# Performance work log

Hardware: AMD Instinct MI355X
Metric: run time of the kernel (lower is better)

## Reference

```python
import jax, jax.numpy as jnp
import numpy as np

B, N, E, D = 2, 4096, 1024, 128  # batch, seq, embed_dim, expand_ratio (head dim)
H = E // D                        # 8 heads
LN_EPS = 1e-5


def setup_inputs() -> dict:
    key = jax.random.key(0)
    ks = jax.random.split(key, 6)
    s = 0.02
    return {
        "x": jax.random.normal(ks[0], (B, N, E), jnp.float32),
        "W_in": jax.random.normal(ks[1], (3 * E, E), jnp.float32) * s,
        "W_out": jax.random.normal(ks[2], (E, E), jnp.float32) * s,
        "W_g1": jax.random.normal(ks[3], (D, E), jnp.float32) * s,
        "W_g2": jax.random.normal(ks[4], (E, D), jnp.float32) * s,
        "ln_w": jnp.ones((E,), jnp.float32),
    }


def _gla_scan(q, k, v, g):
    # q,k,v,g: [b,h,n,d]; GLA recurrence: S_t = exp(g_t)[:,None]*S_{t-1} + k_t v_t^T; o_t = q_t @ S_t
    def step(S, inp):
        qt, kt, vt, gt = inp  # each [b,h,d]
        S = jnp.exp(gt)[..., None] * S + kt[..., None] * vt[..., None, :]  # [b,h,d,d]
        ot = jnp.einsum('bhd,bhde->bhe', qt, S)
        return S, ot

    xs = tuple(jnp.moveaxis(a, 2, 0) for a in (q, k, v, g))  # [n,b,h,d]
    S0 = jnp.zeros(q.shape[:2] + (q.shape[-1], v.shape[-1]), q.dtype)
    _, o = jax.lax.scan(step, S0, xs)
    return jnp.moveaxis(o, 0, 2)  # [b,h,n,d]


def reference(x, W_in, W_out, W_g1, W_g2, ln_w):
    b, n, e = x.shape
    u = x @ W_in.T                       # [b,n,3E]
    v, q, lg = jnp.split(u, 3, axis=-1)  # note order: v, q, log_f
    q = jax.nn.silu(q)                   # q_activation = silu
    f = jax.nn.sigmoid(lg)
    k = 1.0 - f                          # non_sparse_ratio == 1 path
    g = jax.nn.log_sigmoid(lg)           # log of forget gate

    def tohead(a):
        return a.reshape(b, n, H, D).transpose(0, 2, 1, 3)  # b h n d

    o = _gla_scan(tohead(q), tohead(k), tohead(v), tohead(g))
    o = o.transpose(0, 2, 1, 3).reshape(b, n, e)  # b n (h d)

    gate = jax.nn.sigmoid((x @ W_g1.T) @ W_g2.T)  # low-rank output gate
    o = o * gate

    mu = jnp.mean(o, axis=-1, keepdims=True)
    var = jnp.var(o, axis=-1, keepdims=True)
    o = (o - mu) * jax.lax.rsqrt(var + LN_EPS) * ln_w  # layernorm, no bias
    return o @ W_out.T
```

## Files before the change

kernel.cpp:

```cpp
#include <hip/hip_runtime.h>
#include <cmath>

#define B_ 2
#define N_ 4096
#define E_ 1024
#define D_ 128
#define H_ 8
#define CHUNK 64
#define NC_ (N_/CHUNK)
#define UW_ (3*E_ + D_)

__device__ __forceinline__ float sigmoidf_(float x){ return 1.f/(1.f + __expf(-x)); }

__device__ __forceinline__ unsigned short f2bf(float f){
    unsigned u = __float_as_uint(f);
    u += 0x7FFFu + ((u >> 16) & 1u);
    return (unsigned short)(u >> 16);
}
__device__ __forceinline__ float bf2f(unsigned short s){
    return __uint_as_float(((unsigned)s) << 16);
}
__device__ __forceinline__ unsigned short f2bf_fast(float f){
    __bf16 h = (__bf16)f;
    return __builtin_bit_cast(unsigned short, h);
}

typedef __attribute__((ext_vector_type(8))) __bf16 bf16x8;
typedef __attribute__((ext_vector_type(4))) float  f32x4;
typedef __attribute__((address_space(3))) unsigned int as3_u32;
typedef __attribute__((address_space(1))) unsigned int as1_u32;

__device__ __forceinline__ void gload_lds16(const void* g, void* l){
    __builtin_amdgcn_global_load_lds((as1_u32*)g, (as3_u32*)l, 16, 0, 0);
}

__device__ __forceinline__ bf16x8 ldsfrag256(const unsigned short* Lp, int row, int kg){
    return *reinterpret_cast<const bf16x8*>(&Lp[row*128 + ((kg ^ (row&7))<<3)]);
}
__device__ __forceinline__ bf16x8 ldsfrag128(const unsigned short* Lp, int row, int kg){
    return *reinterpret_cast<const bf16x8*>(&Lp[row*64 + ((kg ^ (row&7))<<3)]);
}
__device__ __forceinline__ bf16x8 u4_to_bf(uint4 u){
    return __builtin_bit_cast(bf16x8, u);
}

template<bool OUT_BF16>
__global__ __launch_bounds__(256) void gemm_bf16(
    const unsigned short* __restrict__ A,
    const unsigned short* __restrict__ Bw,
    void* __restrict__ Cout, int M, int N, int K, int lda)
{
    __shared__ unsigned short As[128*64];
    __shared__ unsigned short Bs[128*64];
    const int tid  = threadIdx.x;
    const int wave = tid >> 6;
    const int lane = tid & 63;
    const int gx = gridDim.x;
    const int nwg = gx * gridDim.y;
    int bid = blockIdx.y*gx + blockIdx.x;
    bid = (bid & 7)*(nwg >> 3) + (bid >> 3);
    const int m0 = (bid / gx) * 128, n0 = (bid % gx) * 128;
    const int wr = (wave >> 1) * 64;
    const int wc = (wave & 1) * 64;
    const int l15 = lane & 15, l4 = lane >> 4;
    const int p = l15 & 7;

    f32x4 acc[4][4];
#pragma unroll
    for (int i=0;i<4;i++)
#pragma unroll
        for (int j=0;j<4;j++)
#pragma unroll
            for (int q=0;q<4;q++) acc[i][j][q]=0.f;

    const int srow = wave*32 + (lane>>3);
    const int sgrp = lane & 7;

    for (int k0=0; k0<K; k0+=64){
        if (k0) __syncthreads();
#pragma unroll
        for (int i=0;i<4;i++){
            const int r  = srow + 8*i;
            const int cg = sgrp ^ (r & 7);
            gload_lds16(A  + (size_t)(m0 + r)*lda + k0 + cg*8, &As[(wave*32 + 8*i)*64]);
            gload_lds16(Bw + (size_t)(n0 + r)*K   + k0 + cg*8, &Bs[(wave*32 + 8*i)*64]);
        }
        __syncthreads();
#pragma unroll
        for (int ks=0; ks<2; ks++){
            bf16x8 av[4], bv[4];
            const int tA = (((ks<<2) | l4) ^ p) << 3;
#pragma unroll
            for (int f=0; f<4; f++){
                const int rowA = wr + f*16 + l15;
                const int rowB = wc + f*16 + l15;
                av[f] = *reinterpret_cast<const bf16x8*>(&As[(rowA<<6) + tA]);
                bv[f] = *reinterpret_cast<const bf16x8*>(&Bs[(rowB<<6) + tA]);
            }
#pragma unroll
            for (int fm=0; fm<4; fm++)
#pragma unroll
                for (int fn=0; fn<4; fn++)
                    acc[fm][fn] = __builtin_amdgcn_mfma_f32_16x16x32_bf16(
                        av[fm], bv[fn], acc[fm][fn], 0, 0, 0);
        }
    }
    const int crow0 = m0 + wr + l4*4;
    const int ccol0 = n0 + wc + l15;
    if (!OUT_BF16){
        float* C = (float*)Cout;
#pragma unroll
        for (int fm=0; fm<4; fm++)
#pragma unroll
            for (int fn=0; fn<4; fn++)
#pragma unroll
                for (int j=0;j<4;j++)
                    C[(size_t)(crow0 + fm*16 + j)*N + ccol0 + fn*16] = acc[fm][fn][j];
    } else {
        unsigned short* C = (unsigned short*)Cout;
#pragma unroll
        for (int fm=0; fm<4; fm++)
#pragma unroll
            for (int fn=0; fn<4; fn++)
#pragma unroll
                for (int j=0;j<4;j++)
                    C[(size_t)(crow0 + fm*16 + j)*N + ccol0 + fn*16] = f2bf(acc[fm][fn][j]);
    }
}

#define CQX 2097152
#define WQ1 786432
#define WQ3 32768
#define WQ2 262144
#define WQ4 32768
__global__ __launch_bounds__(256) void cast_all(
    const float* __restrict__ x,
    const float* __restrict__ w1, const float* __restrict__ w3,
    const float* __restrict__ w2, const float* __restrict__ w4,
    unsigned short* __restrict__ xb, unsigned short* __restrict__ wcat,
    unsigned short* __restrict__ w2b, unsigned short* __restrict__ w4b)
{
    const int total = CQX+WQ1+WQ3+WQ2+WQ4;
    for (int i = blockIdx.x*256 + threadIdx.x; i < total; i += gridDim.x*256){
        const float* src; unsigned short* dst; int off;
        if (i < CQX){ src=x; dst=xb; off=i; }
        else if (i < CQX+WQ1){ src=w1; dst=wcat; off=i-CQX; }
        else if (i < CQX+WQ1+WQ3){ src=w3; dst=wcat+WQ1*4; off=i-CQX-WQ1; }
        else if (i < CQX+WQ1+WQ3+WQ2){ src=w2; dst=w2b; off=i-CQX-WQ1-WQ3; }
        else { src=w4; dst=w4b; off=i-CQX-WQ1-WQ3-WQ2; }
        const float4 v = reinterpret_cast<const float4*>(src)[off];
        ushort4 o;
        o.x = f2bf(v.x); o.y = f2bf(v.y); o.z = f2bf(v.z); o.w = f2bf(v.w);
        reinterpret_cast<ushort4*>(dst)[off] = o;
    }
}

__global__ __launch_bounds__(512) void gla_prep(
    const unsigned short* __restrict__ u, float* __restrict__ EBC,
    unsigned short* __restrict__ QSb, unsigned short* __restrict__ KINb,
    unsigned short* __restrict__ KINtb, unsigned short* __restrict__ Vtb)
{
    __shared__ float tot[4*128];
    const int bid = blockIdx.x;
    const int c  = bid % NC_;
    const int hh = (bid / NC_) % H_;
    const int b  = bid / (NC_*H_);
    const int d  = threadIdx.x & 127;
    const int qd = threadIdx.x >> 7;
    const int t0 = qd*16;
    const size_t urow0 = ((size_t)b*N_ + (size_t)c*CHUNK)*UW_ + (size_t)hh*D_ + d;

    float bl[16], qv[16], vv[16];
#pragma unroll
    for (int i=0;i<16;i++)
        bl[i] = bf2f(u[urow0 + (size_t)(t0+i)*UW_ + 2*E_]);
#pragma unroll
    for (int i=0;i<16;i++)
        qv[i] = bf2f(u[urow0 + (size_t)(t0+i)*UW_ + E_]);
#pragma unroll
    for (int i=0;i<16;i++)
        vv[i] = bf2f(u[urow0 + (size_t)(t0+i)*UW_]);

    float acc = 0.f;
#pragma unroll
    for (int i=0;i<16;i++){
        const float lg = bl[i];
        const float e  = __expf(-fabsf(lg));
        const float g  = fminf(lg, 0.f) - __logf(1.f + e);
        acc += g;
        bl[i] = acc;
    }
    tot[qd*128 + d] = acc;
    __syncthreads();
    const float s0 = tot[d], s1 = tot[128+d], s2 = tot[256+d], s3 = tot[384+d];
    const float off = (qd>0 ? s0 : 0.f) + (qd>1 ? s1 : 0.f) + (qd>2 ? s2 : 0.f);
    const float bcv = s0 + s1 + s2 + s3;
    const float ebc = __expf(bcv);
    if (threadIdx.x < 128) EBC[(size_t)bid*D_ + d] = ebc;

    unsigned kin_pk[8], v_pk[8];
    float prev = 0.f;
    const size_t obase = (size_t)bid*CHUNK*D_;
#pragma unroll
    for (int i=0;i<16;i++){
        const int t = t0 + i;
        const float Bl = bl[i];
        const float g  = Bl - prev;  prev = Bl;
        const float Bc = Bl + off;
        const float kk = 1.f - __expf(g);
        const float eB = __expf(Bc);
        const float q  = qv[i];
        const float es = __expf(-q);
        const float silu = q * __builtin_amdgcn_rcpf(1.f + es);
        const float qs  = silu * eB;
        const float kin = kk * __builtin_amdgcn_rcpf(eB);
        QSb [obase + (size_t)t*D_ + d] = f2bf_fast(qs);
        KINb[obase + (size_t)t*D_ + d] = f2bf_fast(kin);
        const unsigned kb = f2bf_fast(kin * ebc);
        const unsigned vb = f2bf_fast(vv[i]);
        if (i & 1){ kin_pk[i>>1] |= kb<<16; v_pk[i>>1] |= vb<<16; }
        else      { kin_pk[i>>1]  = kb;     v_pk[i>>1]  = vb;     }
    }
    const size_t tbase = (size_t)bid*D_*CHUNK + (size_t)d*CHUNK + t0;
#pragma unroll
    for (int j=0;j<2;j++){
        uint4 kq, vq;
        kq.x=kin_pk[4*j]; kq.y=kin_pk[4*j+1]; kq.z=kin_pk[4*j+2]; kq.w=kin_pk[4*j+3];
        vq.x=v_pk[4*j];   vq.y=v_pk[4*j+1];   vq.z=v_pk[4*j+2];   vq.w=v_pk[4*j+3];
        *reinterpret_cast<uint4*>(&KINtb[tbase + j*8]) = kq;
        *reinterpret_cast<uint4*>(&Vtb  [tbase + j*8]) = vq;
    }
}

__global__ __launch_bounds__(256) void gla_chunk_mm(
    const unsigned short* __restrict__ Vtb,
    const unsigned short* __restrict__ KINtb,
    unsigned short* __restrict__ McTb)
{
    __shared__ unsigned short As[128*64];
    __shared__ unsigned short Bs[128*64];
    const int bid = blockIdx.x;
    const int tid = threadIdx.x;
    const int w = tid >> 6, lane = tid & 63;
    const int l15 = lane & 15, l4 = lane >> 4;
    const int wr = (w >> 1) * 64, wc = (w & 1) * 64;
    const unsigned short* A  = Vtb   + (size_t)bid*128*64;
    const unsigned short* Bp = KINtb + (size_t)bid*128*64;

    f32x4 acc[4][4];
#pragma unroll
    for (int i=0;i<4;i++)
#pragma unroll
        for (int j=0;j<4;j++)
#pragma unroll
            for (int q=0;q<4;q++) acc[i][j][q]=0.f;

#pragma unroll
    for (int i=0;i<4;i++){
        const int r  = w*32 + i*8 + (lane>>3);
        const int gs = (lane&7) ^ (r&7);
        gload_lds16(A  + (size_t)r*64 + gs*8, &As[(w*32+i*8)*64]);
        gload_lds16(Bp + (size_t)r*64 + gs*8, &Bs[(w*32+i*8)*64]);
    }
    __syncthreads();
#pragma unroll
    for (int ks=0; ks<2; ks++){
        bf16x8 av[4], bv[4];
#pragma unroll
        for (int f=0; f<4; f++){
            av[f] = ldsfrag128(As, wr + f*16 + l15, ks*4 + l4);
            bv[f] = ldsfrag128(Bs, wc + f*16 + l15, ks*4 + l4);
        }
#pragma unroll
        for (int fm=0; fm<4; fm++)
#pragma unroll
            for (int fn=0; fn<4; fn++)
                acc[fm][fn] = __builtin_amdgcn_mfma_f32_16x16x32_bf16(
                    av[fm], bv[fn], acc[fm][fn], 0, 0, 0);
    }
    unsigned short* C = McTb + (size_t)bid*128*128;
#pragma unroll
    for (int fm=0; fm<4; fm++)
#pragma unroll
        for (int fn=0; fn<4; fn++)
#pragma unroll
            for (int j=0;j<4;j++)
                C[(size_t)(wr + fm*16 + l4*4 + j)*128 + wc + fn*16 + l15] = f2bf(acc[fm][fn][j]);
}

__global__ __launch_bounds__(256) void gla_scan_chunks(
    const unsigned short* __restrict__ McTb, const float* __restrict__ EBC,
    unsigned short* __restrict__ Sb16)
{
    const size_t F = (size_t)blockIdx.x*256 + threadIdx.x;
    const int bh = (int)(F >> 14);
    const int rem = (int)(F & 16383);
    const int d = rem & 127;
    float S = 0.f;
    for (int c=0;c<NC_;c++){
        const size_t idx = (((size_t)bh*NC_ + c) << 14) + rem;
        const float m = bf2f(McTb[idx]);
        const float dec = EBC[((size_t)bh*NC_ + c)*D_ + d];
        Sb16[idx] = f2bf(S);
        S = dec*S + m;
    }
}

__global__ __launch_bounds__(256) void gla_output(
    const unsigned short* __restrict__ QSb,
    const unsigned short* __restrict__ KINb,
    const unsigned short* __restrict__ Vtb,
    const unsigned short* __restrict__ Sb,
    const unsigned short* __restrict__ G2b,
    unsigned short* __restrict__ Opre)
{
    __shared__ unsigned short QS_l[64*128];
    __shared__ unsigned short A_l [64*64];
    const int bid = blockIdx.x;
    const int c = bid % NC_;
    const int h = (bid / NC_) % H_;
    const int b = bid / (NC_*H_);
    const int tid = threadIdx.x;
    const int w = tid >> 6, lane = tid & 63;
    const int l15 = lane & 15, l4 = lane >> 4;

    const unsigned short* qb = QSb + (size_t)bid*64*128;
    const unsigned short* kb = KINb + (size_t)bid*64*128;
    const unsigned short* vb = Vtb + (size_t)bid*128*64;
    const unsigned short* sb = Sb  + (size_t)bid*128*128;

#pragma unroll
    for (int i=0;i<4;i++){
        const int r  = w*16 + i*4 + (lane>>4);
        const int gs = (lane&15) ^ (r&7);
        gload_lds16(qb + (size_t)r*128 + gs*8, &QS_l[(w*16+i*4)*128]);
    }
    uint4 kinr[4];
    {
        const int srow = w*16 + l15;
#pragma unroll
        for (int ks=0; ks<4; ks++)
            kinr[ks] = *reinterpret_cast<const uint4*>(kb + (size_t)srow*128 + (ks*4 + l4)*8);
    }
    __syncthreads();

    uint4 vtr[2][2], sr[2][4];
#pragma unroll
    for (int fe=0; fe<2; fe++){
        const int row = w*32 + fe*16 + l15;
#pragma unroll
        for (int ks=0; ks<2; ks++)
            vtr[fe][ks] = *reinterpret_cast<const uint4*>(vb + (size_t)row*64 + (ks*4 + l4)*8);
#pragma unroll
        for (int ks=0; ks<4; ks++)
            sr[fe][ks]  = *reinterpret_cast<const uint4*>(sb + (size_t)row*128 + (ks*4 + l4)*8);
    }

    f32x4 accA[4];
#pragma unroll
    for (int i=0;i<4;i++)
#pragma unroll
        for (int q=0;q<4;q++) accA[i][q]=0.f;
#pragma unroll
    for (int ks=0; ks<4; ks++){
        const bf16x8 bv = u4_to_bf(kinr[ks]);
#pragma unroll
        for (int ft=0; ft<4; ft++){
            const bf16x8 av = ldsfrag256(QS_l, ft*16 + l15, ks*4 + l4);
            accA[ft] = __builtin_amdgcn_mfma_f32_16x16x32_bf16(av, bv, accA[ft], 0,0,0);
        }
    }
#pragma unroll
    for (int ft=0; ft<4; ft++)
#pragma unroll
        for (int j=0;j<4;j++){
            const int t = ft*16 + l4*4 + j;
            const int s = w*16 + l15;
            const float vA = (t >= s) ? accA[ft][j] : 0.f;
            A_l[t*64 + (((s>>3) ^ (t&7))<<3) + (s&7)] = f2bf(vA);
        }
    __syncthreads();

    f32x4 acc[4][2];
#pragma unroll
    for (int i=0;i<4;i++)
#pragma unroll
        for (int j=0;j<2;j++)
#pragma unroll
            for (int q=0;q<4;q++) acc[i][j][q]=0.f;
#pragma unroll
    for (int ks=0; ks<2; ks++){
        const bf16x8 b0 = u4_to_bf(vtr[0][ks]);
        const bf16x8 b1 = u4_to_bf(vtr[1][ks]);
#pragma unroll
        for (int ft=0; ft<4; ft++){
            const bf16x8 av = ldsfrag128(A_l, ft*16 + l15, ks*4 + l4);
            acc[ft][0] = __builtin_amdgcn_mfma_f32_16x16x32_bf16(av, b0, acc[ft][0], 0,0,0);
            acc[ft][1] = __builtin_amdgcn_mfma_f32_16x16x32_bf16(av, b1, acc[ft][1], 0,0,0);
        }
    }
#pragma unroll
    for (int ks=0; ks<4; ks++){
        const bf16x8 b0 = u4_to_bf(sr[0][ks]);
        const bf16x8 b1 = u4_to_bf(sr[1][ks]);
#pragma unroll
        for (int ft=0; ft<4; ft++){
            const bf16x8 av = ldsfrag256(QS_l, ft*16 + l15, ks*4 + l4);
            acc[ft][0] = __builtin_amdgcn_mfma_f32_16x16x32_bf16(av, b0, acc[ft][0], 0,0,0);
            acc[ft][1] = __builtin_amdgcn_mfma_f32_16x16x32_bf16(av, b1, acc[ft][1], 0,0,0);
        }
    }
    const size_t rowbase = (size_t)b*N_ + (size_t)c*CHUNK;
#pragma unroll
    for (int ft=0; ft<4; ft++)
#pragma unroll
        for (int fe=0; fe<2; fe++)
#pragma unroll
            for (int j=0;j<4;j++){
                const int t = ft*16 + l4*4 + j;
                const int e = w*32 + fe*16 + l15;
                const size_t idx = (rowbase + t)*E_ + h*D_ + e;
                const float g = sigmoidf_(bf2f(G2b[idx]));
                Opre[idx] = f2bf(acc[ft][fe][j] * g);
            }
}

__global__ __launch_bounds__(256) void ln_bf16(
    const unsigned short* __restrict__ O, const float* __restrict__ lnw,
    unsigned short* __restrict__ Ob)
{
    const int row = blockIdx.x;
    const int tid = threadIdx.x;
    const size_t off = (size_t)row*E_ + tid*4;
    const ushort4 ov = *reinterpret_cast<const ushort4*>(&O[off]);
    float4 o;
    o.x = bf2f(ov.x); o.y = bf2f(ov.y); o.z = bf2f(ov.z); o.w = bf2f(ov.w);
    float s1 = o.x+o.y+o.z+o.w;
    float s2 = o.x*o.x + o.y*o.y + o.z*o.z + o.w*o.w;
#pragma unroll
    for (int sh=32; sh>0; sh>>=1){
        s1 += __shfl_down(s1, sh);
        s2 += __shfl_down(s2, sh);
    }
    __shared__ float r1[4], r2[4];
    const int wid = tid >> 6;
    if ((tid & 63)==0){ r1[wid]=s1; r2[wid]=s2; }
    __syncthreads();
    s1 = r1[0]+r1[1]+r1[2]+r1[3];
    s2 = r2[0]+r2[1]+r2[2]+r2[3];
    const float mean = s1 * (1.f/E_);
    const float var  = s2 * (1.f/E_) - mean*mean;
    const float rs   = rsqrtf(var + 1e-5f);
    const float4 w = *reinterpret_cast<const float4*>(&lnw[tid*4]);
    ushort4 r;
    r.x = f2bf((o.x-mean)*rs*w.x); r.y = f2bf((o.y-mean)*rs*w.y);
    r.z = f2bf((o.z-mean)*rs*w.z); r.w = f2bf((o.w-mean)*rs*w.w);
    *reinterpret_cast<ushort4*>(&Ob[off]) = r;
}

extern "C" void kernel_launch(void* const* d_in, const int* in_sizes, int n_in,
                              void* d_out, int out_size, void* d_ws, size_t ws_size,
                              hipStream_t stream)
{
    const float* x     = (const float*)d_in[0];
    const float* W_in  = (const float*)d_in[1];
    const float* W_out = (const float*)d_in[2];
    const float* W_g1  = (const float*)d_in[3];
    const float* W_g2  = (const float*)d_in[4];
    const float* lnw   = (const float*)d_in[5];
    float* out = (float*)d_out;
    char* ws = (char*)d_ws;

    unsigned short* ub2    = (unsigned short*)(ws);
    unsigned short* McTb   = (unsigned short*)(ws);
    unsigned short* Sb16   = (unsigned short*)(ws + 33554432);
    unsigned short* G2b    = (unsigned short*)(ws + 67108864);
    float*          EBC    = (float*)(ws + 100663296);
    unsigned short* QSb    = (unsigned short*)(ws + 101187584);
    unsigned short* KINb   = (unsigned short*)(ws + 117964800);
    unsigned short* KINtb  = (unsigned short*)(ws + 134742016);
    unsigned short* Vtb    = (unsigned short*)(ws + 151519232);
    unsigned short* Opre   = (unsigned short*)(ws + 168296448);
    unsigned short* xb     = (unsigned short*)(ws + 185073664);
    unsigned short* Wcatb  = (unsigned short*)(ws + 201850880);
    unsigned short* W_outb = (unsigned short*)(ws + 224919552);
    unsigned short* W_g2b  = (unsigned short*)(ws + 227278848);
    unsigned short* ObF    = (unsigned short*)(ws + 229638144);

    const int M = B_*N_;
    dim3 blk(256);

    cast_all<<<2048, blk, 0, stream>>>(x, W_in, W_g1, W_out, W_g2,
                                       xb, Wcatb, W_outb, W_g2b);

    gemm_bf16<true><<<dim3(UW_/128, M/128), blk, 0, stream>>>(
        xb, Wcatb, ub2, M, UW_, E_, E_);
    gla_prep<<<dim3(B_*H_*NC_), dim3(512), 0, stream>>>(ub2, EBC, QSb, KINb, KINtb, Vtb);
    gemm_bf16<true><<<dim3(E_/128, M/128), blk, 0, stream>>>(
        ub2 + 3*E_, W_g2b, G2b, M, E_, D_, UW_);
    gla_chunk_mm<<<dim3(B_*H_*NC_), blk, 0, stream>>>(Vtb, KINtb, McTb);
    gla_scan_chunks<<<dim3((B_*H_*D_*D_)/256), blk, 0, stream>>>(McTb, EBC, Sb16);
    gla_output<<<dim3(B_*H_*NC_), blk, 0, stream>>>(QSb, KINb, Vtb, Sb16, G2b, Opre);
    ln_bf16<<<dim3(M), blk, 0, stream>>>(Opre, lnw, ObF);
    gemm_bf16<false><<<dim3(E_/128, M/128), blk, 0, stream>>>(
        ObF, W_outb, out, M, E_, E_, E_);
}
```

Before: 195.0 us.

## Fuse low-rank gate GEMM into GLA output kernel and vectorize chunk scan

Removes the separate gate GEMM that wrote a bf16 gate tensor. The gla_output kernel now computes the gate's second projection in place with MFMA, reading the rank-128 projection from ub2 and W_g2. The chunk scan kernel now handles four state elements per thread with vector loads and stores, using a quarter of the blocks. The workspace is relaid out so ub2 is no longer aliased by McTb, since ub2 must survive until gla_output; this adds per-block MFMA work and uncoalesced global fragment loads.

```diff
diff --git a/kernel.cpp b/kernel.cpp
--- a/kernel.cpp
+++ b/kernel.cpp
@@ -292,17 +292,24 @@
     const unsigned short* __restrict__ McTb, const float* __restrict__ EBC,
     unsigned short* __restrict__ Sb16)
 {
-    const size_t F = (size_t)blockIdx.x*256 + threadIdx.x;
-    const int bh = (int)(F >> 14);
-    const int rem = (int)(F & 16383);
-    const int d = rem & 127;
-    float S = 0.f;
+    const int F4 = blockIdx.x*256 + threadIdx.x;
+    const int e4 = F4 << 2;
+    const int bh = e4 >> 14;
+    const int rem = e4 & 16383;
+    const int d0 = rem & 127;
+    float S0=0.f, S1=0.f, S2=0.f, S3=0.f;
     for (int c=0;c<NC_;c++){
         const size_t idx = (((size_t)bh*NC_ + c) << 14) + rem;
-        const float m = bf2f(McTb[idx]);
-        const float dec = EBC[((size_t)bh*NC_ + c)*D_ + d];
-        Sb16[idx] = f2bf(S);
-        S = dec*S + m;
+        const ushort4 m4 = *reinterpret_cast<const ushort4*>(&McTb[idx]);
+        const float4 dec = *reinterpret_cast<const float4*>(
+            &EBC[(((size_t)bh*NC_ + c) << 7) + d0]);
+        ushort4 s4;
+        s4.x = f2bf(S0); s4.y = f2bf(S1); s4.z = f2bf(S2); s4.w = f2bf(S3);
+        *reinterpret_cast<ushort4*>(&Sb16[idx]) = s4;
+        S0 = dec.x*S0 + bf2f(m4.x);
+        S1 = dec.y*S1 + bf2f(m4.y);
+        S2 = dec.z*S2 + bf2f(m4.z);
+        S3 = dec.w*S3 + bf2f(m4.w);
     }
 }
 
@@ -311,7 +318,8 @@
     const unsigned short* __restrict__ KINb,
     const unsigned short* __restrict__ Vtb,
     const unsigned short* __restrict__ Sb,
-    const unsigned short* __restrict__ G2b,
+    const unsigned short* __restrict__ ub2,
+    const unsigned short* __restrict__ Wg2,
     unsigned short* __restrict__ Opre)
 {
     __shared__ unsigned short QS_l[64*128];
@@ -328,6 +336,7 @@
     const unsigned short* kb = KINb + (size_t)bid*64*128;
     const unsigned short* vb = Vtb + (size_t)bid*128*64;
     const unsigned short* sb = Sb  + (size_t)bid*128*128;
+    const size_t rowbase = (size_t)b*N_ + (size_t)c*CHUNK;
 
 #pragma unroll
     for (int i=0;i<4;i++){
@@ -410,7 +419,33 @@
             acc[ft][1] = __builtin_amdgcn_mfma_f32_16x16x32_bf16(av, b1, acc[ft][1], 0,0,0);
         }
     }
-    const size_t rowbase = (size_t)b*N_ + (size_t)c*CHUNK;
+
+    f32x4 acc2[4][2];
+#pragma unroll
+    for (int i=0;i<4;i++)
+#pragma unroll
+        for (int j=0;j<2;j++)
+#pragma unroll
+            for (int q=0;q<4;q++) acc2[i][j][q]=0.f;
+#pragma unroll
+    for (int ks=0; ks<4; ks++){
+        const int kq = (ks*4 + l4)*8;
+        bf16x8 bg[2], ag[4];
+#pragma unroll
+        for (int fe=0; fe<2; fe++)
+            bg[fe] = *reinterpret_cast<const bf16x8*>(
+                &Wg2[(size_t)(h*128 + w*32 + fe*16 + l15)*D_ + kq]);
+#pragma unroll
+        for (int ft=0; ft<4; ft++)
+            ag[ft] = *reinterpret_cast<const bf16x8*>(
+                &ub2[(rowbase + ft*16 + l15)*UW_ + 3*E_ + kq]);
+#pragma unroll
+        for (int ft=0; ft<4; ft++){
+            acc2[ft][0] = __builtin_amdgcn_mfma_f32_16x16x32_bf16(ag[ft], bg[0], acc2[ft][0], 0,0,0);
+            acc2[ft][1] = __builtin_amdgcn_mfma_f32_16x16x32_bf16(ag[ft], bg[1], acc2[ft][1], 0,0,0);
+        }
+    }
+
 #pragma unroll
     for (int ft=0; ft<4; ft++)
 #pragma unroll
@@ -420,7 +455,7 @@
                 const int t = ft*16 + l4*4 + j;
                 const int e = w*32 + fe*16 + l15;
                 const size_t idx = (rowbase + t)*E_ + h*D_ + e;
-                const float g = sigmoidf_(bf2f(G2b[idx]));
+                const float g = sigmoidf_(acc2[ft][fe][j]);
                 Opre[idx] = f2bf(acc[ft][fe][j] * g);
             }
 }
@@ -472,20 +507,19 @@
     char* ws = (char*)d_ws;
 
     unsigned short* ub2    = (unsigned short*)(ws);
-    unsigned short* McTb   = (unsigned short*)(ws);
-    unsigned short* Sb16   = (unsigned short*)(ws + 33554432);
-    unsigned short* G2b    = (unsigned short*)(ws + 67108864);
-    float*          EBC    = (float*)(ws + 100663296);
-    unsigned short* QSb    = (unsigned short*)(ws + 101187584);
-    unsigned short* KINb   = (unsigned short*)(ws + 117964800);
-    unsigned short* KINtb  = (unsigned short*)(ws + 134742016);
-    unsigned short* Vtb    = (unsigned short*)(ws + 151519232);
-    unsigned short* Opre   = (unsigned short*)(ws + 168296448);
-    unsigned short* xb     = (unsigned short*)(ws + 185073664);
-    unsigned short* Wcatb  = (unsigned short*)(ws + 201850880);
-    unsigned short* W_outb = (unsigned short*)(ws + 224919552);
-    unsigned short* W_g2b  = (unsigned short*)(ws + 227278848);
-    unsigned short* ObF    = (unsigned short*)(ws + 229638144);
+    unsigned short* QSb    = (unsigned short*)(ws + 52428800);
+    unsigned short* KINb   = (unsigned short*)(ws + 69206016);
+    unsigned short* KINtb  = (unsigned short*)(ws + 85983232);
+    unsigned short* Vtb    = (unsigned short*)(ws + 102760448);
+    unsigned short* McTb   = (unsigned short*)(ws + 119537664);
+    unsigned short* Sb16   = (unsigned short*)(ws + 153092096);
+    float*          EBC    = (float*)(ws + 186646528);
+    unsigned short* Opre   = (unsigned short*)(ws + 187170816);
+    unsigned short* ObF    = (unsigned short*)(ws + 203948032);
+    unsigned short* xb     = (unsigned short*)(ws + 220725248);
+    unsigned short* Wcatb  = (unsigned short*)(ws + 237502464);
+    unsigned short* W_outb = (unsigned short*)(ws + 244056064);
+    unsigned short* W_g2b  = (unsigned short*)(ws + 246153216);
 
     const int M = B_*N_;
     dim3 blk(256);
@@ -496,11 +530,9 @@
     gemm_bf16<true><<<dim3(UW_/128, M/128), blk, 0, stream>>>(
         xb, Wcatb, ub2, M, UW_, E_, E_);
     gla_prep<<<dim3(B_*H_*NC_), dim3(512), 0, stream>>>(ub2, EBC, QSb, KINb, KINtb, Vtb);
-    gemm_bf16<true><<<dim3(E_/128, M/128), blk, 0, stream>>>(
-        ub2 + 3*E_, W_g2b, G2b, M, E_, D_, UW_);
     gla_chunk_mm<<<dim3(B_*H_*NC_), blk, 0, stream>>>(Vtb, KINtb, McTb);
-    gla_scan_chunks<<<dim3((B_*H_*D_*D_)/256), blk, 0, stream>>>(McTb, EBC, Sb16);
-    gla_output<<<dim3(B_*H_*NC_), blk, 0, stream>>>(QSb, KINb, Vtb, Sb16, G2b, Opre);
+    gla_scan_chunks<<<dim3((B_*H_*D_*D_)/1024), blk, 0, stream>>>(McTb, EBC, Sb16);
+    gla_output<<<dim3(B_*H_*NC_), blk, 0, stream>>>(QSb, KINb, Vtb, Sb16, ub2, W_g2b, Opre);
     ln_bf16<<<dim3(M), blk, 0, stream>>>(Opre, lnw, ObF);
     gemm_bf16<false><<<dim3(E_/128, M/128), blk, 0, stream>>>(
         ObF, W_outb, out, M, E_, E_, E_);
```

Measured after the change: 196.2 us. About the same (+0.6%).

## Use 256x256 eight-phase pipelined GEMM for input projection

Applied to the files above, without the earlier changes.

Adds a 512-thread GEMM kernel with 256x256 output tiles. It uses 128 KB of LDS and splits each K-step into quarter-tile phases that interleave direct global-to-LDS loads with MFMA work, separated by barriers and s_setprio. UW_ is padded from 3200 to 3328 so the width divides evenly by 256, and the workspace layout is rearranged to fit the wider buffer. The aim is more data reuse and better load/compute overlap on the largest GEMM. The cost is padding compute, only 416 blocks, and heavy register and LDS pressure.

```diff
diff --git a/kernel.cpp b/kernel.cpp
--- a/kernel.cpp
+++ b/kernel.cpp
@@ -8,7 +8,7 @@
 #define H_ 8
 #define CHUNK 64
 #define NC_ (N_/CHUNK)
-#define UW_ (3*E_ + D_)
+#define UW_ 3328
 
 __device__ __forceinline__ float sigmoidf_(float x){ return 1.f/(1.f + __expf(-x)); }
 
@@ -42,6 +42,138 @@
 }
 __device__ __forceinline__ bf16x8 u4_to_bf(uint4 u){
     return __builtin_bit_cast(bf16x8, u);
+}
+
+template<bool OUT_BF16>
+__global__ __launch_bounds__(512) void gemm_8ph(
+    const unsigned short* __restrict__ Ag,
+    const unsigned short* __restrict__ Bg,
+    void* __restrict__ Cout, int M, int N, int K, int lda, int ldc)
+{
+    __shared__ unsigned short LDS8[65536];
+    const int tid  = threadIdx.x;
+    const int wave = tid >> 6;
+    const int lane = tid & 63;
+    const int l15 = lane & 15, l4 = lane >> 4;
+    const int wm = wave >> 2, wn = wave & 3;
+
+    const int gx = gridDim.x;
+    const int nwg = gx * gridDim.y;
+    int bid = blockIdx.y*gx + blockIdx.x;
+    bid = (bid & 7)*(nwg >> 3) + (bid >> 3);
+    const int m0 = (bid / gx) * 256, n0 = (bid % gx) * 256;
+
+    f32x4 acc[8][4];
+#pragma unroll
+    for (int i=0;i<8;i++)
+#pragma unroll
+        for (int j=0;j<4;j++)
+#pragma unroll
+            for (int q=0;q<4;q++) acc[i][j][q]=0.f;
+
+    bf16x8 a[4][2], b[2][2];
+
+    auto STAGE_A = [&](int kt, int buf, int h){
+        unsigned short* dst = &LDS8[(buf*2+h)*8192];
+        const int k0 = kt*64;
+#pragma unroll
+        for (int j=0;j<2;j++){
+            const int R = j*64 + wave*8 + (lane>>3);
+            const int trow = j*128 + h*64 + (R&63);
+            gload_lds16(Ag + (size_t)(m0+trow)*lda + k0 + (((lane&7) ^ (R&7))<<3),
+                        dst + (j*64 + wave*8)*64);
+        }
+    };
+    auto STAGE_B = [&](int kt, int buf, int h){
+        unsigned short* dst = &LDS8[32768 + (buf*2+h)*8192];
+        const int k0 = kt*64;
+#pragma unroll
+        for (int j=0;j<2;j++){
+            const int R = j*64 + wave*8 + (lane>>3);
+            const int tcol = (R>>5)*64 + h*32 + (R&31);
+            gload_lds16(Bg + (size_t)(n0+tcol)*K + k0 + (((lane&7) ^ (R&7))<<3),
+                        dst + (j*64 + wave*8)*64);
+        }
+    };
+
+#define RD_A(BUF, MQ) { _Pragma("unroll") for (int f_=0;f_<4;f_++) _Pragma("unroll") \
+    for (int k_=0;k_<2;k_++) a[f_][k_] = ldsfrag128(&LDS8[((BUF)*2+(MQ))*8192], wm*64 + f_*16 + l15, k_*4 + l4); }
+#define RD_B(BUF, NQ) { _Pragma("unroll") for (int f_=0;f_<2;f_++) _Pragma("unroll") \
+    for (int k_=0;k_<2;k_++) b[f_][k_] = ldsfrag128(&LDS8[32768 + ((BUF)*2+(NQ))*8192], wn*32 + f_*16 + l15, k_*4 + l4); }
+#define MMQ(MQ, NQ) { __builtin_amdgcn_s_setprio(1); _Pragma("unroll") \
+    for (int k_=0;k_<2;k_++) _Pragma("unroll") for (int f_=0;f_<4;f_++) _Pragma("unroll") \
+    for (int g_=0;g_<2;g_++) acc[(MQ)*4+f_][(NQ)*2+g_] = __builtin_amdgcn_mfma_f32_16x16x32_bf16( \
+        a[f_][k_], b[g_][k_], acc[(MQ)*4+f_][(NQ)*2+g_], 0,0,0); __builtin_amdgcn_s_setprio(0); }
+#define BAR1() { __builtin_amdgcn_s_barrier(); \
+    asm volatile("s_waitcnt lgkmcnt(0)" ::: "memory"); __builtin_amdgcn_sched_barrier(0); }
+#define BAR2() { __builtin_amdgcn_s_barrier(); __builtin_amdgcn_sched_barrier(0); }
+#define VM6BAR() { asm volatile("s_waitcnt vmcnt(6)" ::: "memory"); \
+    __builtin_amdgcn_s_barrier(); __builtin_amdgcn_sched_barrier(0); }
+
+    STAGE_A(0,0,0); STAGE_B(0,0,0); STAGE_B(0,0,1); STAGE_A(0,0,1);
+    STAGE_A(1,1,0); STAGE_B(1,1,1); STAGE_A(1,1,1);
+    asm volatile("s_waitcnt vmcnt(0)" ::: "memory");
+    BAR2();
+
+    const int NT = K >> 6;
+    for (int i=0; i<(NT>>1); ++i){
+        const int t1 = 2*i+1;
+        const int t2 = (2*i+2 < NT) ? 2*i+2 : 0;
+        const int t3 = (2*i+3 < NT) ? 2*i+3 : 0;
+        RD_A(0,0); RD_B(0,0); STAGE_B(t1, 1, 0);
+        BAR1(); MMQ(0,0); BAR2();
+        RD_B(0,1); STAGE_A(t2, 0, 0);
+        BAR1(); MMQ(0,1); BAR2();
+        RD_A(0,1); STAGE_B(t2, 0, 1);
+        BAR1(); MMQ(1,1); BAR2();
+        RD_B(0,0); STAGE_A(t2, 0, 1);
+        BAR1(); MMQ(1,0); VM6BAR();
+        RD_A(1,0); RD_B(1,0); STAGE_B(t2, 0, 0);
+        BAR1(); MMQ(0,0); BAR2();
+        RD_B(1,1); STAGE_A(t3, 1, 0);
+        BAR1(); MMQ(0,1); BAR2();
+        RD_A(1,1); STAGE_B(t3, 1, 1);
+        BAR1(); MMQ(1,1); BAR2();
+        RD_B(1,0); STAGE_A(t3, 1, 1);
+        BAR1(); MMQ(1,0); VM6BAR();
+    }
+    asm volatile("s_waitcnt vmcnt(0)" ::: "memory");
+#undef RD_A
+#undef RD_B
+#undef MMQ
+#undef BAR1
+#undef BAR2
+#undef VM6BAR
+
+    if (!OUT_BF16){
+        float* C = (float*)Cout;
+#pragma unroll
+        for (int mq=0; mq<2; mq++)
+#pragma unroll
+            for (int f=0; f<4; f++)
+#pragma unroll
+                for (int nq=0; nq<2; nq++)
+#pragma unroll
+                    for (int g=0; g<2; g++)
+#pragma unroll
+                        for (int j=0;j<4;j++)
+                            C[(size_t)(m0 + wm*128 + mq*64 + f*16 + l4*4 + j)*ldc
+                              + n0 + wn*64 + nq*32 + g*16 + l15] = acc[mq*4+f][nq*2+g][j];
+    } else {
+        unsigned short* C = (unsigned short*)Cout;
+#pragma unroll
+        for (int mq=0; mq<2; mq++)
+#pragma unroll
+            for (int f=0; f<4; f++)
+#pragma unroll
+                for (int nq=0; nq<2; nq++)
+#pragma unroll
+                    for (int g=0; g<2; g++)
+#pragma unroll
+                        for (int j=0;j<4;j++)
+                            C[(size_t)(m0 + wm*128 + mq*64 + f*16 + l4*4 + j)*ldc
+                              + n0 + wn*64 + nq*32 + g*16 + l15] = f2bf(acc[mq*4+f][nq*2+g][j]);
+    }
 }
 
 template<bool OUT_BF16>
@@ -473,19 +605,19 @@
 
     unsigned short* ub2    = (unsigned short*)(ws);
     unsigned short* McTb   = (unsigned short*)(ws);
-    unsigned short* Sb16   = (unsigned short*)(ws + 33554432);
-    unsigned short* G2b    = (unsigned short*)(ws + 67108864);
-    float*          EBC    = (float*)(ws + 100663296);
-    unsigned short* QSb    = (unsigned short*)(ws + 101187584);
-    unsigned short* KINb   = (unsigned short*)(ws + 117964800);
-    unsigned short* KINtb  = (unsigned short*)(ws + 134742016);
-    unsigned short* Vtb    = (unsigned short*)(ws + 151519232);
-    unsigned short* Opre   = (unsigned short*)(ws + 168296448);
-    unsigned short* xb     = (unsigned short*)(ws + 185073664);
-    unsigned short* Wcatb  = (unsigned short*)(ws + 201850880);
-    unsigned short* W_outb = (unsigned short*)(ws + 224919552);
-    unsigned short* W_g2b  = (unsigned short*)(ws + 227278848);
-    unsigned short* ObF    = (unsigned short*)(ws + 229638144);
+    unsigned short* QSb    = (unsigned short*)(ws + 54525952);
+    unsigned short* KINb   = (unsigned short*)(ws + 71303168);
+    unsigned short* KINtb  = (unsigned short*)(ws + 88080384);
+    unsigned short* Vtb    = (unsigned short*)(ws + 104857600);
+    unsigned short* Sb16   = (unsigned short*)(ws + 121634816);
+    float*          EBC    = (float*)(ws + 155189248);
+    unsigned short* Opre   = (unsigned short*)(ws + 155713536);
+    unsigned short* ObF    = (unsigned short*)(ws + 172490752);
+    unsigned short* xb     = (unsigned short*)(ws + 189267968);
+    unsigned short* G2b    = (unsigned short*)(ws + 189267968);
+    unsigned short* Wcatb  = (unsigned short*)(ws + 206045184);
+    unsigned short* W_outb = (unsigned short*)(ws + 212860928);
+    unsigned short* W_g2b  = (unsigned short*)(ws + 214958080);
 
     const int M = B_*N_;
     dim3 blk(256);
@@ -493,8 +625,8 @@
     cast_all<<<2048, blk, 0, stream>>>(x, W_in, W_g1, W_out, W_g2,
                                        xb, Wcatb, W_outb, W_g2b);
 
-    gemm_bf16<true><<<dim3(UW_/128, M/128), blk, 0, stream>>>(
-        xb, Wcatb, ub2, M, UW_, E_, E_);
+    gemm_8ph<true><<<dim3(UW_/256, M/256), dim3(512), 0, stream>>>(
+        xb, Wcatb, ub2, M, UW_, E_, E_, UW_);
     gla_prep<<<dim3(B_*H_*NC_), dim3(512), 0, stream>>>(ub2, EBC, QSb, KINb, KINtb, Vtb);
     gemm_bf16<true><<<dim3(E_/128, M/128), blk, 0, stream>>>(
         ub2 + 3*E_, W_g2b, G2b, M, E_, D_, UW_);
```

New measurement: 190.0 us. -2.6%, faster.
